# Performance work log

Hardware: AMD Instinct MI355X
Metric: run time of the kernel (lower is better)

Reference implementation:

```python
import jax, jax.numpy as jnp
import numpy as np

B, S, H, Q = 32, 128, 128, 3  # users, seq_len, hidden_size, quadkey_level
L = Q - 1  # number of mixing scales


def setup_inputs() -> dict:
    key = jax.random.key(0)
    ks = jax.random.split(key, 12)
    trend0 = jax.random.normal(ks[0], (B, S, H), dtype=jnp.float32)
    trend1 = jax.random.normal(ks[1], (B, S, H), dtype=jnp.float32)
    trend2 = jax.random.normal(ks[2], (B, S, H), dtype=jnp.float32)
    # Per-position prefix linears padded into dense tensors, zero-masked beyond
    # the prefix length j+1 so the ragged math is exact:
    #   W1[j, :j+1, :j+1] ~ Linear(j+1, j+1), b1[j, :j+1]
    #   W2[j, :j+1]      ~ Linear(j+1, 1),   b2[j]
    idx = jnp.arange(S)
    pm = (idx[None, :] <= idx[:, None]).astype(jnp.float32)  # [j, s]: s <= j
    W1 = jax.random.normal(ks[3], (L, S, S, S), dtype=jnp.float32) * 0.05
    W1 = W1 * pm[None, :, :, None] * pm[None, :, None, :]
    b1 = jax.random.normal(ks[4], (L, S, S), dtype=jnp.float32) * 0.05 * pm[None]
    W2 = jax.random.normal(ks[5], (L, S, S), dtype=jnp.float32) * 0.05 * pm[None]
    b2 = jax.random.normal(ks[6], (L, S), dtype=jnp.float32) * 0.05
    # shared output MLP: Linear(H,H)->GELU->Linear(H,H); stored as [in, out]
    Wm1 = jax.random.normal(ks[7], (H, H), dtype=jnp.float32) * 0.05
    bm1 = jax.random.normal(ks[8], (H,), dtype=jnp.float32) * 0.05
    Wm2 = jax.random.normal(ks[9], (H, H), dtype=jnp.float32) * 0.05
    bm2 = jax.random.normal(ks[10], (H,), dtype=jnp.float32) * 0.05
    return {"trend0": trend0, "trend1": trend1, "trend2": trend2,
            "W1": W1, "b1": b1, "W2": W2, "b2": b2,
            "Wm1": Wm1, "bm1": bm1, "Wm2": Wm2, "bm2": bm2}


def reference(trend0, trend1, trend2, W1, b1, W2, b2, Wm1, bm1, Wm2, bm2):
    gelu = lambda x: jax.nn.gelu(x, approximate=False)  # torch nn.GELU default
    mlp = lambda x: gelu(x @ Wm1 + bm1) @ Wm2 + bm2

    rev = [trend2, trend1, trend0]  # trend_list reversed
    out_low = rev[0]
    out_high = rev[1]
    outs = [out_low]
    for i in range(Q - 1):
        # vectorized ragged prefix mix: per position j, out_low[:, :j+1] (as [B,H,j+1])
        # -> Linear(j+1,j+1) -> GELU -> Linear(j+1,1). Zero-padding in W1/b1/W2
        # kills all contributions beyond the prefix (GELU(0)=0).
        y1 = jnp.einsum('bsh,jst->bhjt', out_low, W1[i]) + b1[i]  # [B,H,S,S]
        res = jnp.einsum('bhjt,jt->bjh', gelu(y1), W2[i]) + b2[i][None, :, None]
        out_high = out_high + res
        out_low = out_high
        if i + 2 <= Q - 1:
            out_high = rev[i + 2]
        out_low = mlp(out_low)
        outs.append(out_low)
    outs.reverse()
    return tuple(outs)
```

## Files before the change

kernel.cpp:

```cpp
#include <hip/hip_runtime.h>
#include <stdint.h>

#define BSH (32 * 128 * 128)

typedef __attribute__((ext_vector_type(8))) __bf16 bf16x8;
typedef __attribute__((ext_vector_type(4))) float f32x4;

__device__ __forceinline__ unsigned short f2bf(float f) {
  union { float f; unsigned u; } v; v.f = f;
  return (unsigned short)((v.u + 0x7FFFu + ((v.u >> 16) & 1u)) >> 16);
}

__device__ __forceinline__ float fast_exp2(float x) {
#if __has_builtin(__builtin_amdgcn_exp2f)
  return __builtin_amdgcn_exp2f(x);
#else
  float r; asm("v_exp_f32 %0, %1" : "=v"(r) : "v"(x)); return r;
#endif
}
__device__ __forceinline__ float fast_rcp(float x) {
#if __has_builtin(__builtin_amdgcn_rcpf)
  return __builtin_amdgcn_rcpf(x);
#else
  float r; asm("v_rcp_f32 %0, %1" : "=v"(r) : "v"(x)); return r;
#endif
}

__device__ __forceinline__ float gelu_f(float y) {
  float u = y * y;
  float p = __builtin_fmaf(u, 0.044715f, 1.0f) * y;
  float w = fast_exp2(p * 2.30220787f);
  return y - y * fast_rcp(1.0f + w);
}

__device__ __forceinline__ void transpose_block_c(const float* __restrict__ src,
                                                  unsigned short* __restrict__ dst,
                                                  unsigned short* lds) {
  const int tid = threadIdx.x;
  const float4* s4 = (const float4*)src;
#pragma unroll
  for (int it = 0; it < 16; ++it) {
    int i4 = tid + it * 256;
    float4 v = s4[i4];
    int s = i4 >> 5;
    int t0 = (i4 * 4) & 127;
    int sc = s >> 3, se = s & 7;
#pragma unroll
    for (int e = 0; e < 4; ++e) {
      int t = t0 + e;
      lds[t * 136 + ((sc ^ ((t >> 2) & 7)) << 3) + se] = f2bf(((const float*)&v)[e]);
    }
  }
  __syncthreads();
#pragma unroll
  for (int it = 0; it < 8; ++it) {
    int c = tid + it * 256;
    int tr = c >> 4, sc = c & 15;
    uint4 d = *(const uint4*)(lds + tr * 136 + ((sc ^ ((tr >> 2) & 7)) << 3));
    *(uint4*)(dst + (sc * 128 + tr) * 8) = d;
  }
}

__global__ __launch_bounds__(256) void prepass_kernel(
    const float* __restrict__ W1, const float* __restrict__ trend2,
    const float* __restrict__ Wm1, const float* __restrict__ Wm2,
    unsigned short* __restrict__ W1Tc, unsigned short* __restrict__ T2c,
    unsigned short* __restrict__ Wm1c, unsigned short* __restrict__ Wm2c,
    float* __restrict__ out2) {
  __shared__ unsigned short lds[128 * 136];
  const int bid = blockIdx.x;
  if (bid < 256) {
    int x = bid & 7, i = bid >> 3;
    int stage = i >> 4, u = i & 15;
    int m = u & 7, half = u >> 3;
    int jpp = x + 8 * m;
    int j = half ? 127 - jpp : jpp;
    int blk = stage * 128 + j;
    transpose_block_c(W1 + blk * 16384, W1Tc + blk * 16384, lds);
  } else if (bid < 288) {
    const int b = bid - 256;
    transpose_block_c(trend2 + b * 16384, T2c + b * 16384, lds);
    const float4* s4 = (const float4*)(trend2 + b * 16384);
    float4* d4 = (float4*)(out2 + b * 16384);
#pragma unroll
    for (int it = 0; it < 16; ++it)
      d4[threadIdx.x + it * 256] = s4[threadIdx.x + it * 256];
  } else if (bid == 288) {
    transpose_block_c(Wm1, Wm1c, lds);
  } else {
    transpose_block_c(Wm2, Wm2c, lds);
  }
}

__global__ __launch_bounds__(128, 4) void mix_kernel(
    const unsigned short* __restrict__ XTc,
    const unsigned short* __restrict__ W1Tj,
    const float* __restrict__ b1j,
    const float* __restrict__ W2j,
    const float* __restrict__ b2j,
    const float* __restrict__ trendR,
    unsigned short* __restrict__ xoutc) {
  const int bid = blockIdx.x;
  const int b = bid >> 6;
  const int jp = bid & 63;
  const int js = jp, jb = 127 - jp;
  const int tid = threadIdx.x;
  const int p = tid >> 6;
  const int lane = tid & 63;
  const int lane15 = lane & 15;
  const int quad = lane >> 4;

  const int nt_s = (js >> 4) + 1, ks_s = (js >> 5) + 1;
  const int nt_b = (jb >> 4) + 1, ks_b = (jb >> 5) + 1;

  const unsigned short* Bp = XTc + b * 16384 + (p * 64 + lane15) * 8;
  const unsigned short* As = W1Tj + js * 16384 + lane15 * 8;
  const unsigned short* Ab = W1Tj + jb * 16384 + lane15 * 8;
  const float C = -2.45546937f;

  float psum[2][4];
#pragma unroll
  for (int jj = 0; jj < 2; ++jj)
#pragma unroll
    for (int ni = 0; ni < 4; ++ni) psum[jj][ni] = 0.f;

  for (int mt = 0; mt < nt_b; ++mt) {
    const bool in_s = (mt < nt_s);
    f32x4 acc[2][4];
#pragma unroll
    for (int jj = 0; jj < 2; ++jj)
#pragma unroll
      for (int ni = 0; ni < 4; ++ni) {
        f32x4 z = {0.f, 0.f, 0.f, 0.f};
        acc[jj][ni] = z;
      }
    const int mo = mt * 128;
    for (int ks = 0; ks < ks_b; ++ks) {
      const int ko = (ks * 4 + quad) * 1024;
      bf16x8 vb0 = *(const bf16x8*)(Bp + ko);
      bf16x8 vb1 = *(const bf16x8*)(Bp + ko + 128);
      bf16x8 vb2 = *(const bf16x8*)(Bp + ko + 256);
      bf16x8 vb3 = *(const bf16x8*)(Bp + ko + 384);
      bf16x8 ab = *(const bf16x8*)(Ab + ko + mo);
      acc[1][0] = __builtin_amdgcn_mfma_f32_16x16x32_bf16(ab, vb0, acc[1][0], 0, 0, 0);
      acc[1][1] = __builtin_amdgcn_mfma_f32_16x16x32_bf16(ab, vb1, acc[1][1], 0, 0, 0);
      acc[1][2] = __builtin_amdgcn_mfma_f32_16x16x32_bf16(ab, vb2, acc[1][2], 0, 0, 0);
      acc[1][3] = __builtin_amdgcn_mfma_f32_16x16x32_bf16(ab, vb3, acc[1][3], 0, 0, 0);
      if (in_s && ks < ks_s) {
        bf16x8 as = *(const bf16x8*)(As + ko + mo);
        acc[0][0] = __builtin_amdgcn_mfma_f32_16x16x32_bf16(as, vb0, acc[0][0], 0, 0, 0);
        acc[0][1] = __builtin_amdgcn_mfma_f32_16x16x32_bf16(as, vb1, acc[0][1], 0, 0, 0);
        acc[0][2] = __builtin_amdgcn_mfma_f32_16x16x32_bf16(as, vb2, acc[0][2], 0, 0, 0);
        acc[0][3] = __builtin_amdgcn_mfma_f32_16x16x32_bf16(as, vb3, acc[0][3], 0, 0, 0);
      }
    }
    const int tb = mt * 16 + quad * 4;
#pragma unroll
    for (int jj = 0; jj < 2; ++jj) {
      if (jj == 0 && !in_s) continue;
      const int j = jj ? jb : js;
      float4 b1v = *(const float4*)(b1j + j * 128 + tb);
      float4 w2v = *(const float4*)(W2j + j * 128 + tb);
#pragma unroll
      for (int r = 0; r < 4; ++r) {
        float b1r = ((const float*)&b1v)[r];
        float w2r = ((const float*)&w2v)[r];
        float cb = C * b1r;
        float bw = b1r * w2r;
#pragma unroll
        for (int ni = 0; ni < 4; ++ni) {
          float a = acc[jj][ni][r];
          float m = __builtin_fmaf(a, C, cb);
          float e = fast_exp2(m);
          float rr2 = fast_rcp(1.0f + e);
          float yw = __builtin_fmaf(a, w2r, bw);
          psum[jj][ni] = __builtin_fmaf(yw, rr2, psum[jj][ni]);
        }
      }
    }
  }

#pragma unroll
  for (int jj = 0; jj < 2; ++jj)
#pragma unroll
    for (int ni = 0; ni < 4; ++ni) {
      float v = psum[jj][ni];
      v += __shfl_xor(v, 16, 64);
      v += __shfl_xor(v, 32, 64);
      psum[jj][ni] = v;
    }

  if (quad == 0) {
#pragma unroll
    for (int jj = 0; jj < 2; ++jj) {
      const int j = jj ? jb : js;
      const float bias = b2j[j];
#pragma unroll
      for (int ni = 0; ni < 4; ++ni) {
        const int h = p * 64 + ni * 16 + lane15;
        float v = psum[jj][ni] + bias + trendR[(b * 128 + j) * 128 + h];
        xoutc[b * 16384 + ((h >> 3) * 128 + j) * 8 + (h & 7)] = f2bf(v);
      }
    }
  }
}

__global__ __launch_bounds__(256) void mlp_kernel(
    const unsigned short* __restrict__ Xc,
    const unsigned short* __restrict__ Wm1c,
    const unsigned short* __restrict__ Wm2c,
    const float* __restrict__ bm1,
    const float* __restrict__ bm2,
    float* __restrict__ outf,
    unsigned short* __restrict__ outTc,
    const int write_t) {
  __shared__ __align__(16) unsigned short U[16 * 128];
  __shared__ unsigned short ldsT[16 * 136];
  const int bid = blockIdx.x;
  const int b = bid >> 3;
  const int mb = bid & 7;
  const int tid = threadIdx.x;
  const int wave = tid >> 6;
  const int lane = tid & 63;
  const int lane15 = lane & 15;
  const int quad = lane >> 4;

  const unsigned short* Xb = Xc + b * 16384;

  f32x4 acc[2];
  { f32x4 z = {0.f, 0.f, 0.f, 0.f}; acc[0] = z; acc[1] = z; }
#pragma unroll
  for (int ks = 0; ks < 4; ++ks) {
    int kq = ks * 4 + quad;
    bf16x8 a  = *(const bf16x8*)(Xb + (kq * 128 + mb * 16 + lane15) * 8);
    bf16x8 w0 = *(const bf16x8*)(Wm1c + (kq * 128 + wave * 32 + lane15) * 8);
    bf16x8 w1 = *(const bf16x8*)(Wm1c + (kq * 128 + wave * 32 + 16 + lane15) * 8);
    acc[0] = __builtin_amdgcn_mfma_f32_16x16x32_bf16(a, w0, acc[0], 0, 0, 0);
    acc[1] = __builtin_amdgcn_mfma_f32_16x16x32_bf16(a, w1, acc[1], 0, 0, 0);
  }
#pragma unroll
  for (int ni = 0; ni < 2; ++ni) {
    int n = wave * 32 + ni * 16 + lane15;
    float bv = bm1[n];
#pragma unroll
    for (int r = 0; r < 4; ++r) {
      int jr = quad * 4 + r;
      U[((n >> 3) * 16 + jr) * 8 + (n & 7)] = f2bf(gelu_f(acc[ni][r] + bv));
    }
  }
  __syncthreads();
  { f32x4 z = {0.f, 0.f, 0.f, 0.f}; acc[0] = z; acc[1] = z; }
#pragma unroll
  for (int ks = 0; ks < 4; ++ks) {
    int kq = ks * 4 + quad;
    bf16x8 a  = *(const bf16x8*)(U + (kq * 16 + lane15) * 8);
    bf16x8 w0 = *(const bf16x8*)(Wm2c + (kq * 128 + wave * 32 + lane15) * 8);
    bf16x8 w1 = *(const bf16x8*)(Wm2c + (kq * 128 + wave * 32 + 16 + lane15) * 8);
    acc[0] = __builtin_amdgcn_mfma_f32_16x16x32_bf16(a, w0, acc[0], 0, 0, 0);
    acc[1] = __builtin_amdgcn_mfma_f32_16x16x32_bf16(a, w1, acc[1], 0, 0, 0);
  }
  {
    float* outb = outf + b * 16384 + mb * 16 * 128;
#pragma unroll
    for (int ni = 0; ni < 2; ++ni) {
      int n = wave * 32 + ni * 16 + lane15;
      float bv = bm2[n];
#pragma unroll
      for (int r = 0; r < 4; ++r) {
        int jr = quad * 4 + r;
        float v = acc[ni][r] + bv;
        outb[jr * 128 + n] = v;
        if (write_t) ldsT[jr * 136 + n] = f2bf(v);
      }
    }
  }
  if (write_t) {
    __syncthreads();
    int h = tid & 127, jr8 = tid >> 7;
    unsigned short tmp[8] __attribute__((aligned(16)));
#pragma unroll
    for (int e = 0; e < 8; ++e) tmp[e] = ldsT[(jr8 * 8 + e) * 136 + h];
    *(uint4*)(outTc + b * 16384 + ((mb * 2 + jr8) * 128 + h) * 8) = *(const uint4*)tmp;
  }
}

extern "C" void kernel_launch(void* const* d_in, const int* in_sizes, int n_in,
                              void* d_out, int out_size, void* d_ws, size_t ws_size,
                              hipStream_t stream) {
  (void)in_sizes; (void)n_in; (void)out_size; (void)ws_size;
  const float* trend0 = (const float*)d_in[0];
  const float* trend1 = (const float*)d_in[1];
  const float* trend2 = (const float*)d_in[2];
  const float* W1  = (const float*)d_in[3];
  const float* b1  = (const float*)d_in[4];
  const float* W2  = (const float*)d_in[5];
  const float* b2  = (const float*)d_in[6];
  const float* Wm1 = (const float*)d_in[7];
  const float* bm1 = (const float*)d_in[8];
  const float* Wm2 = (const float*)d_in[9];
  const float* bm2 = (const float*)d_in[10];
  float* out = (float*)d_out;
  char* ws = (char*)d_ws;

  unsigned short* W1Tc = (unsigned short*)(ws);
  unsigned short* T2c  = (unsigned short*)(ws + 8388608);
  unsigned short* x1c  = (unsigned short*)(ws + 9437184);
  unsigned short* A1Tc = (unsigned short*)(ws + 10485760);
  unsigned short* x2c  = (unsigned short*)(ws + 11534336);
  unsigned short* Wm1c = (unsigned short*)(ws + 12582912);
  unsigned short* Wm2c = (unsigned short*)(ws + 12615680);

  prepass_kernel<<<290, 256, 0, stream>>>(W1, trend2, Wm1, Wm2,
                                          W1Tc, T2c, Wm1c, Wm2c, out + 2 * BSH);
  mix_kernel<<<2048, 128, 0, stream>>>(T2c, W1Tc, b1, W2, b2, trend1, x1c);
  mlp_kernel<<<256, 256, 0, stream>>>(x1c, Wm1c, Wm2c, bm1, bm2,
                                      out + BSH, A1Tc, 1);
  mix_kernel<<<2048, 128, 0, stream>>>(A1Tc, W1Tc + 128 * 16384, b1 + 16384,
                                       W2 + 16384, b2 + 128, trend0, x2c);
  mlp_kernel<<<256, 256, 0, stream>>>(x2c, Wm1c, Wm2c, bm1, bm2,
                                      out, (unsigned short*)nullptr, 0);
}
```

Measured before the change: 152.7 us.

## Preload activation fragments into registers and split big/small prefix loops

Loads the X^T B-operand fragments for all k-steps into registers once per block instead of reloading them on every m-tile. The fused loop that handled both the long and short prefix positions is split into two separate loops, which removes the per-iteration in_s branch and fully unrolls the k loop. Holding 16 bf16x8 vectors raises register pressure, so the occupancy hint in launch_bounds is lowered from 4 to 3. The main risk is lower occupancy, which may expose more memory latency.

After: 138.5 us. 9.3% less time.

```diff
diff --git a/kernel.cpp b/kernel.cpp
--- a/kernel.cpp
+++ b/kernel.cpp
@@ -92,7 +92,7 @@
   }
 }
 
-__global__ __launch_bounds__(128, 4) void mix_kernel(
+__global__ __launch_bounds__(128, 3) void mix_kernel(
     const unsigned short* __restrict__ XTc,
     const unsigned short* __restrict__ W1Tj,
     const float* __restrict__ b1j,
@@ -118,6 +118,17 @@
   const unsigned short* Ab = W1Tj + jb * 16384 + lane15 * 8;
   const float C = -2.45546937f;
 
+  bf16x8 Bv[4][4];
+#pragma unroll
+  for (int ks = 0; ks < 4; ++ks)
+    if (ks < ks_b) {
+      const int ko = (ks * 4 + quad) * 1024;
+      Bv[ks][0] = *(const bf16x8*)(Bp + ko);
+      Bv[ks][1] = *(const bf16x8*)(Bp + ko + 128);
+      Bv[ks][2] = *(const bf16x8*)(Bp + ko + 256);
+      Bv[ks][3] = *(const bf16x8*)(Bp + ko + 384);
+    }
+
   float psum[2][4];
 #pragma unroll
   for (int jj = 0; jj < 2; ++jj)
@@ -125,57 +136,71 @@
     for (int ni = 0; ni < 4; ++ni) psum[jj][ni] = 0.f;
 
   for (int mt = 0; mt < nt_b; ++mt) {
-    const bool in_s = (mt < nt_s);
-    f32x4 acc[2][4];
-#pragma unroll
-    for (int jj = 0; jj < 2; ++jj)
+    f32x4 acc[4];
+#pragma unroll
+    for (int ni = 0; ni < 4; ++ni) { f32x4 z = {0.f, 0.f, 0.f, 0.f}; acc[ni] = z; }
+    const int mo = mt * 128;
+#pragma unroll
+    for (int ks = 0; ks < 4; ++ks)
+      if (ks < ks_b) {
+        bf16x8 a = *(const bf16x8*)(Ab + (ks * 4 + quad) * 1024 + mo);
+        acc[0] = __builtin_amdgcn_mfma_f32_16x16x32_bf16(a, Bv[ks][0], acc[0], 0, 0, 0);
+        acc[1] = __builtin_amdgcn_mfma_f32_16x16x32_bf16(a, Bv[ks][1], acc[1], 0, 0, 0);
+        acc[2] = __builtin_amdgcn_mfma_f32_16x16x32_bf16(a, Bv[ks][2], acc[2], 0, 0, 0);
+        acc[3] = __builtin_amdgcn_mfma_f32_16x16x32_bf16(a, Bv[ks][3], acc[3], 0, 0, 0);
+      }
+    const int tb = mt * 16 + quad * 4;
+    float4 b1v = *(const float4*)(b1j + jb * 128 + tb);
+    float4 w2v = *(const float4*)(W2j + jb * 128 + tb);
+#pragma unroll
+    for (int r = 0; r < 4; ++r) {
+      float b1r = ((const float*)&b1v)[r];
+      float w2r = ((const float*)&w2v)[r];
+      float cb = C * b1r;
+      float bw = b1r * w2r;
 #pragma unroll
       for (int ni = 0; ni < 4; ++ni) {
-        f32x4 z = {0.f, 0.f, 0.f, 0.f};
-        acc[jj][ni] = z;
-      }
+        float a = acc[ni][r];
+        float m = __builtin_fmaf(a, C, cb);
+        float e = fast_exp2(m);
+        float rr2 = fast_rcp(1.0f + e);
+        float yw = __builtin_fmaf(a, w2r, bw);
+        psum[1][ni] = __builtin_fmaf(yw, rr2, psum[1][ni]);
+      }
+    }
+  }
+
+  for (int mt = 0; mt < nt_s; ++mt) {
+    f32x4 acc[4];
+#pragma unroll
+    for (int ni = 0; ni < 4; ++ni) { f32x4 z = {0.f, 0.f, 0.f, 0.f}; acc[ni] = z; }
     const int mo = mt * 128;
-    for (int ks = 0; ks < ks_b; ++ks) {
-      const int ko = (ks * 4 + quad) * 1024;
-      bf16x8 vb0 = *(const bf16x8*)(Bp + ko);
-      bf16x8 vb1 = *(const bf16x8*)(Bp + ko + 128);
-      bf16x8 vb2 = *(const bf16x8*)(Bp + ko + 256);
-      bf16x8 vb3 = *(const bf16x8*)(Bp + ko + 384);
-      bf16x8 ab = *(const bf16x8*)(Ab + ko + mo);
-      acc[1][0] = __builtin_amdgcn_mfma_f32_16x16x32_bf16(ab, vb0, acc[1][0], 0, 0, 0);
-      acc[1][1] = __builtin_amdgcn_mfma_f32_16x16x32_bf16(ab, vb1, acc[1][1], 0, 0, 0);
-      acc[1][2] = __builtin_amdgcn_mfma_f32_16x16x32_bf16(ab, vb2, acc[1][2], 0, 0, 0);
-      acc[1][3] = __builtin_amdgcn_mfma_f32_16x16x32_bf16(ab, vb3, acc[1][3], 0, 0, 0);
-      if (in_s && ks < ks_s) {
-        bf16x8 as = *(const bf16x8*)(As + ko + mo);
-        acc[0][0] = __builtin_amdgcn_mfma_f32_16x16x32_bf16(as, vb0, acc[0][0], 0, 0, 0);
-        acc[0][1] = __builtin_amdgcn_mfma_f32_16x16x32_bf16(as, vb1, acc[0][1], 0, 0, 0);
-        acc[0][2] = __builtin_amdgcn_mfma_f32_16x16x32_bf16(as, vb2, acc[0][2], 0, 0, 0);
-        acc[0][3] = __builtin_amdgcn_mfma_f32_16x16x32_bf16(as, vb3, acc[0][3], 0, 0, 0);
-      }
-    }
+#pragma unroll
+    for (int ks = 0; ks < 2; ++ks)
+      if (ks < ks_s) {
+        bf16x8 a = *(const bf16x8*)(As + (ks * 4 + quad) * 1024 + mo);
+        acc[0] = __builtin_amdgcn_mfma_f32_16x16x32_bf16(a, Bv[ks][0], acc[0], 0, 0, 0);
+        acc[1] = __builtin_amdgcn_mfma_f32_16x16x32_bf16(a, Bv[ks][1], acc[1], 0, 0, 0);
+        acc[2] = __builtin_amdgcn_mfma_f32_16x16x32_bf16(a, Bv[ks][2], acc[2], 0, 0, 0);
+        acc[3] = __builtin_amdgcn_mfma_f32_16x16x32_bf16(a, Bv[ks][3], acc[3], 0, 0, 0);
+      }
     const int tb = mt * 16 + quad * 4;
-#pragma unroll
-    for (int jj = 0; jj < 2; ++jj) {
-      if (jj == 0 && !in_s) continue;
-      const int j = jj ? jb : js;
-      float4 b1v = *(const float4*)(b1j + j * 128 + tb);
-      float4 w2v = *(const float4*)(W2j + j * 128 + tb);
-#pragma unroll
-      for (int r = 0; r < 4; ++r) {
-        float b1r = ((const float*)&b1v)[r];
-        float w2r = ((const float*)&w2v)[r];
-        float cb = C * b1r;
-        float bw = b1r * w2r;
-#pragma unroll
-        for (int ni = 0; ni < 4; ++ni) {
-          float a = acc[jj][ni][r];
-          float m = __builtin_fmaf(a, C, cb);
-          float e = fast_exp2(m);
-          float rr2 = fast_rcp(1.0f + e);
-          float yw = __builtin_fmaf(a, w2r, bw);
-          psum[jj][ni] = __builtin_fmaf(yw, rr2, psum[jj][ni]);
-        }
+    float4 b1v = *(const float4*)(b1j + js * 128 + tb);
+    float4 w2v = *(const float4*)(W2j + js * 128 + tb);
+#pragma unroll
+    for (int r = 0; r < 4; ++r) {
+      float b1r = ((const float*)&b1v)[r];
+      float w2r = ((const float*)&w2v)[r];
+      float cb = C * b1r;
+      float bw = b1r * w2r;
+#pragma unroll
+      for (int ni = 0; ni < 4; ++ni) {
+        float a = acc[ni][r];
+        float m = __builtin_fmaf(a, C, cb);
+        float e = fast_exp2(m);
+        float rr2 = fast_rcp(1.0f + e);
+        float yw = __builtin_fmaf(a, w2r, bw);
+        psum[0][ni] = __builtin_fmaf(yw, rr2, psum[0][ni]);
       }
     }
   }
```
